# Performance work log

Hardware: AMD Instinct MI355X
Metric: run time of the kernel (lower is better)

The kernel has to match this reference:

```python
import jax, jax.numpy as jnp
import numpy as np

N = 100000
E = 1600000
IN_C = 128
OUT_C = 64
HID = 2 * OUT_C  # 128


def gcn_conv(x, src, dst, W, b, n):
    # PyG GCNConv with add_self_loops=True, symmetric normalization, bias.
    h = x @ W  # [n, d_out] - transform first (PyG order)
    ones = jnp.ones(src.shape[0], dtype=h.dtype)
    deg = jax.ops.segment_sum(ones, dst, num_segments=n)  # includes self-loops -> deg >= 1
    dinv = jax.lax.rsqrt(deg)
    norm = dinv[src] * dinv[dst]  # [E+n]
    msg = h[src] * norm[:, None]  # gather + scale
    return jax.ops.segment_sum(msg, dst, num_segments=n) + b


def setup_inputs() -> dict:
    key = jax.random.key(0)
    ks = jax.random.split(key, 8)
    x = jax.random.normal(ks[0], (N, IN_C), dtype=jnp.float32)
    edge_index = jax.random.randint(ks[1], (2, E), 0, N, dtype=jnp.int64)
    s1 = 1.0 / np.sqrt(IN_C)
    s2 = 1.0 / np.sqrt(HID)
    s3 = 1.0 / np.sqrt(OUT_C)
    W1 = jax.random.normal(ks[2], (IN_C, HID), dtype=jnp.float32) * s1
    b1 = jnp.zeros((HID,), dtype=jnp.float32)
    W2 = jax.random.normal(ks[3], (HID, OUT_C), dtype=jnp.float32) * s2
    b2 = jnp.zeros((OUT_C,), dtype=jnp.float32)
    Wfc = jax.random.normal(ks[4], (OUT_C, OUT_C), dtype=jnp.float32) * s3
    bfc = jax.random.uniform(ks[5], (OUT_C,), dtype=jnp.float32, minval=-s3, maxval=s3)
    return {"x": x, "edge_index": edge_index, "W1": W1, "b1": b1,
            "W2": W2, "b2": b2, "Wfc": Wfc, "bfc": bfc}


def reference(x, edge_index, W1, b1, W2, b2, Wfc, bfc):
    n = x.shape[0]
    loop = jnp.arange(n, dtype=edge_index.dtype)
    src = jnp.concatenate([edge_index[0], loop])  # add self-loops
    dst = jnp.concatenate([edge_index[1], loop])
    h = jax.nn.relu(gcn_conv(x, src, dst, W1, b1, n))
    h = gcn_conv(h, src, dst, W2, b2, n)
    return h @ Wfc + bfc
```

## Files before the change

### kernel.cpp

```cpp
#include <hip/hip_runtime.h>

#define INC  128
#define HIDC 128
#define OUTC 64

#define BSH   8
#define NBMAX 512
#define HB    128
#define TILE  4096
#define CAP   8192

typedef unsigned int  u32;
typedef unsigned short u16;
typedef short bf16x8 __attribute__((ext_vector_type(8)));
typedef float f32x4 __attribute__((ext_vector_type(4)));

static __device__ __forceinline__ u16 f2bf(float f) {
    u32 u = __builtin_bit_cast(u32, f);
    u += 0x7fffu + ((u >> 16) & 1u);
    return (u16)(u >> 16);
}
static __device__ __forceinline__ float bf_lo(u32 u) {
    return __builtin_bit_cast(float, u << 16);
}
static __device__ __forceinline__ float bf_hi(u32 u) {
    return __builtin_bit_cast(float, u & 0xffff0000u);
}


__global__ __launch_bounds__(256) void bhist_kernel(const int* __restrict__ dst,
                                                    int* __restrict__ parts,
                                                    int E, int nb) {
    __shared__ int h[NBMAX];
    for (int i = threadIdx.x; i < NBMAX; i += 256) h[i] = 0;
    __syncthreads();
    const int total = HB * 256;
    for (int e = blockIdx.x * 256 + threadIdx.x; e < E; e += total)
        atomicAdd(&h[dst[e] >> BSH], 1);
    __syncthreads();
    for (int i = threadIdx.x; i < nb; i += 256) parts[i * HB + blockIdx.x] = h[i];
}

__global__ __launch_bounds__(512) void bscan_kernel(const int* __restrict__ parts,
                                                    int* __restrict__ bucketOff, int nb) {
    __shared__ int sums[NBMAX];
    const int tid = threadIdx.x;
    int s = 0;
    if (tid < nb) {
        const int* p = parts + tid * HB;
#pragma unroll 8
        for (int r = 0; r < HB; ++r) s += p[r];
    }
    sums[tid] = s;
    __syncthreads();
    for (int d = 1; d < NBMAX; d <<= 1) {
        int t = sums[tid];
        int a = (tid >= d) ? sums[tid - d] : 0;
        __syncthreads();
        sums[tid] = t + a;
        __syncthreads();
    }
    if (tid < nb) bucketOff[tid] = sums[tid] - s;
    if (tid == NBMAX - 1) bucketOff[nb] = sums[NBMAX - 1];
}

__global__ __launch_bounds__(256) void multisplit_kernel(const int* __restrict__ src,
                                                         const int* __restrict__ dst,
                                                         const int* __restrict__ bucketOff,
                                                         int* __restrict__ gfill,
                                                         int2* __restrict__ binned,
                                                         int E, int nb) {
    __shared__ int hist[NBMAX];
    __shared__ int sbase[NBMAX];
    __shared__ int cursor[NBMAX];
    __shared__ int gposs[NBMAX];
    __shared__ int wsum[4];
    __shared__ int2 buf[TILE];
    const int tid  = threadIdx.x;
    const int base = blockIdx.x * TILE;
    const int cnt  = min(TILE, E - base);

    for (int i = tid; i < NBMAX; i += 256) hist[i] = 0;
    __syncthreads();

    int ls[16], ld[16], dg[16];
#pragma unroll
    for (int k = 0; k < 16; ++k) {
        int idx = tid + k * 256;
        if (idx < cnt) {
            ls[k] = src[base + idx];
            ld[k] = dst[base + idx];
            dg[k] = ld[k] >> BSH;
            atomicAdd(&hist[dg[k]], 1);
        } else dg[k] = -1;
    }
    __syncthreads();
    {
        const int a = hist[2 * tid], b = hist[2 * tid + 1];
        const int s = a + b;
        const int lane = tid & 63;
        int incl = s;
#pragma unroll
        for (int d = 1; d < 64; d <<= 1) {
            int t = __shfl_up(incl, d);
            if (lane >= d) incl += t;
        }
        if (lane == 63) wsum[tid >> 6] = incl;
        __syncthreads();
        const int w = tid >> 6;
        int wbase = 0;
        if (w > 0) wbase += wsum[0];
        if (w > 1) wbase += wsum[1];
        if (w > 2) wbase += wsum[2];
        const int excl = wbase + incl - s;
        sbase[2 * tid] = excl;          cursor[2 * tid] = excl;
        sbase[2 * tid + 1] = excl + a;  cursor[2 * tid + 1] = excl + a;
    }
    __syncthreads();
#pragma unroll
    for (int k = 0; k < 16; ++k) {
        if (dg[k] >= 0) {
            int p = atomicAdd(&cursor[dg[k]], 1);
            buf[p] = make_int2(ls[k], ld[k]);
        }
    }
    __syncthreads();
    for (int d = tid; d < nb; d += 256) {
        int c = cursor[d] - sbase[d];
        gposs[d] = (c > 0) ? atomicAdd(&gfill[d], c) : 0;
    }
    __syncthreads();
    for (int idx = tid; idx < cnt; idx += 256) {
        int2 e = buf[idx];
        int d = e.y >> BSH;
        binned[bucketOff[d] + gposs[d] + (idx - sbase[d])] = e;
    }
}

__global__ __launch_bounds__(256) void csr_build_kernel(const int2* __restrict__ binned,
                                                        const int* __restrict__ bucketOff,
                                                        int* __restrict__ col,
                                                        int* __restrict__ rowptr,
                                                        float* __restrict__ dinv,
                                                        int n, int E) {
    __shared__ int cnt[257];
    __shared__ int excl[256];
    __shared__ int wsum[4];
    __shared__ int colstage[CAP];
    const int tid   = threadIdx.x;
    const int b     = blockIdx.x;
    const int node0 = b << BSH;
    const int nNodes = min(256, n - node0);
    const int e0 = bucketOff[b], e1 = bucketOff[b + 1];
    const int ec = e1 - e0;

    for (int i = tid; i <= 256; i += 256) cnt[i] = 0;
    __syncthreads();
    for (int i = tid; i < ec; i += 256)
        atomicAdd(&cnt[binned[e0 + i].y & 255], 1);
    __syncthreads();
    const int myc = cnt[tid];
    {
        const int lane = tid & 63;
        int incl = myc;
#pragma unroll
        for (int d = 1; d < 64; d <<= 1) {
            int t = __shfl_up(incl, d);
            if (lane >= d) incl += t;
        }
        if (lane == 63) wsum[tid >> 6] = incl;
        __syncthreads();
        const int w = tid >> 6;
        int wbase = 0;
        if (w > 0) wbase += wsum[0];
        if (w > 1) wbase += wsum[1];
        if (w > 2) wbase += wsum[2];
        excl[tid] = wbase + incl - myc;
    }
    __syncthreads();
    if (tid < nNodes) {
        const int node = node0 + tid;
        rowptr[node] = e0 + excl[tid];
        dinv[node] = rsqrtf((float)(myc + 1));
    }
    if (b == 0 && tid == 0) rowptr[n] = E;
    __syncthreads();
    cnt[tid] = excl[tid];
    __syncthreads();
    if (ec <= CAP) {
        for (int i = tid; i < ec; i += 256) {
            int2 e = binned[e0 + i];
            int p = atomicAdd(&cnt[e.y & 255], 1);
            colstage[p] = e.x;
        }
        __syncthreads();
        for (int i = tid; i < ec; i += 256) col[e0 + i] = colstage[i];
    } else {
        for (int i = tid; i < ec; i += 256) {
            int2 e = binned[e0 + i];
            int p = atomicAdd(&cnt[e.y & 255], 1);
            col[e0 + p] = e.x;
        }
    }
}

__global__ __launch_bounds__(256) void fold_kernel(const float* __restrict__ W1,
                                                   const float* __restrict__ W2,
                                                   const float* __restrict__ Wfc,
                                                   const float* __restrict__ b2,
                                                   const float* __restrict__ bfc,
                                                   u16* __restrict__ W1t,
                                                   u16* __restrict__ W2ft,
                                                   float* __restrict__ b2f) {
    int t = blockIdx.x * 256 + threadIdx.x;
    if (t < HIDC * HIDC) {
        int nn = t >> 7, k = t & 127;
        W1t[nn * HIDC + k] = f2bf(W1[k * HIDC + nn]);
    } else if (t < HIDC * HIDC + HIDC * OUTC) {
        int u = t - HIDC * HIDC;
        int i = u >> 6, j = u & 63;
        float s = 0.f;
#pragma unroll 8
        for (int k = 0; k < OUTC; ++k) s = fmaf(W2[i * OUTC + k], Wfc[k * OUTC + j], s);
        W2ft[j * HIDC + i] = f2bf(s);
    } else if (t < HIDC * HIDC + HIDC * OUTC + OUTC) {
        int j = t - HIDC * HIDC - HIDC * OUTC;
        float s = bfc[j];
#pragma unroll 8
        for (int k = 0; k < OUTC; ++k) s = fmaf(b2[k], Wfc[k * OUTC + j], s);
        b2f[j] = s;
    }
}


template <int N, bool AF32>
__global__ __launch_bounds__(256) void mfma_gemm_kernel(const void* __restrict__ Aptr,
                                                        const u16* __restrict__ Wt,
                                                        const float* __restrict__ dinv,
                                                        u16* __restrict__ out, int M) {
    constexpr int K = 128;
    constexpr int NC = N / 16;
    __shared__ u16 Ws[N * K];

    const int tid = threadIdx.x;
    for (int id = tid; id < N * K / 8; id += 256) {
        int nn = id >> 4;
        int c  = id & 15;
        uint4 v = *(const uint4*)(Wt + nn * K + c * 8);
        int slot = (nn << 4) + (c ^ (nn & 7));
        *(uint4*)((char*)Ws + slot * 16) = v;
    }

    const int wave = tid >> 6;
    const int lane = tid & 63;
    const int r0   = blockIdx.x * 64 + wave * 16;
    const int arow = r0 + (lane & 15);
    const int kgrp = lane >> 4;
    __syncthreads();

    f32x4 acc[NC];
#pragma unroll
    for (int nc = 0; nc < NC; ++nc) acc[nc] = f32x4{0.f, 0.f, 0.f, 0.f};

#pragma unroll
    for (int kc = 0; kc < 4; ++kc) {
        bf16x8 af = {0, 0, 0, 0, 0, 0, 0, 0};
        if (arow < M) {
            if constexpr (AF32) {
                const float* ap = (const float*)Aptr + (size_t)arow * K + kc * 32 + kgrp * 8;
                float4 v0 = *(const float4*)ap;
                float4 v1 = *(const float4*)(ap + 4);
                af[0] = (short)f2bf(v0.x); af[1] = (short)f2bf(v0.y);
                af[2] = (short)f2bf(v0.z); af[3] = (short)f2bf(v0.w);
                af[4] = (short)f2bf(v1.x); af[5] = (short)f2bf(v1.y);
                af[6] = (short)f2bf(v1.z); af[7] = (short)f2bf(v1.w);
            } else {
                af = *(const bf16x8*)((const u16*)Aptr + (size_t)arow * K + kc * 32 + kgrp * 8);
            }
        }
#pragma unroll
        for (int nc = 0; nc < NC; ++nc) {
            int nn = nc * 16 + (lane & 15);
            int slot = (nn << 4) + ((kc * 4 + kgrp) ^ (nn & 7));
            bf16x8 bfr = *(const bf16x8*)((const char*)Ws + slot * 16);
            acc[nc] = __builtin_amdgcn_mfma_f32_16x16x32_bf16(af, bfr, acc[nc], 0, 0, 0);
        }
    }
#pragma unroll
    for (int reg = 0; reg < 4; ++reg) {
        int row = r0 + (lane >> 4) * 4 + reg;
        if (row < M) {
            float sc = dinv[row];
#pragma unroll
            for (int nc = 0; nc < NC; ++nc)
                out[(size_t)row * N + nc * 16 + (lane & 15)] = f2bf(acc[nc][reg] * sc);
        }
    }
}


__global__ __launch_bounds__(256) void agg1_kernel(const u32* __restrict__ g,
                                                   const int* __restrict__ rowptr,
                                                   const int* __restrict__ col,
                                                   const float* __restrict__ dinv,
                                                   const float* __restrict__ b1,
                                                   u32* __restrict__ h1, int n) {
    const int wid  = threadIdx.x >> 6;
    const int lane = threadIdx.x & 63;
    const int v = blockIdx.x * 4 + wid;
    if (v >= n) return;
    const int base = rowptr[v], endi = rowptr[v + 1];

    u32 uv = g[(size_t)v * 64 + lane];
    float a0x = bf_lo(uv), a0y = bf_hi(uv);
    float a1x = 0.f, a1y = 0.f, a2x = 0.f, a2y = 0.f, a3x = 0.f, a3y = 0.f;
    float a4x = 0.f, a4y = 0.f, a5x = 0.f, a5y = 0.f, a6x = 0.f, a6y = 0.f, a7x = 0.f, a7y = 0.f;

    for (int c = base; c < endi; c += 64) {
        const int m = min(64, endi - c);
        const int idx = col[c + min(lane, m - 1)];
        for (int i = 0; i < m; i += 8) {
            int u0 = __shfl(idx, i);
            int u1 = __shfl(idx, min(i + 1, m - 1));
            int u2 = __shfl(idx, min(i + 2, m - 1));
            int u3 = __shfl(idx, min(i + 3, m - 1));
            int u4 = __shfl(idx, min(i + 4, m - 1));
            int u5 = __shfl(idx, min(i + 5, m - 1));
            int u6 = __shfl(idx, min(i + 6, m - 1));
            int u7 = __shfl(idx, min(i + 7, m - 1));
            float w1 = (i + 1 < m) ? 1.f : 0.f;
            float w2 = (i + 2 < m) ? 1.f : 0.f;
            float w3 = (i + 3 < m) ? 1.f : 0.f;
            float w4 = (i + 4 < m) ? 1.f : 0.f;
            float w5 = (i + 5 < m) ? 1.f : 0.f;
            float w6 = (i + 6 < m) ? 1.f : 0.f;
            float w7 = (i + 7 < m) ? 1.f : 0.f;
            u32 x0 = g[(size_t)u0 * 64 + lane];
            u32 x1 = g[(size_t)u1 * 64 + lane];
            u32 x2 = g[(size_t)u2 * 64 + lane];
            u32 x3 = g[(size_t)u3 * 64 + lane];
            u32 x4 = g[(size_t)u4 * 64 + lane];
            u32 x5 = g[(size_t)u5 * 64 + lane];
            u32 x6 = g[(size_t)u6 * 64 + lane];
            u32 x7 = g[(size_t)u7 * 64 + lane];
            a0x += bf_lo(x0);                a0y += bf_hi(x0);
            a1x = fmaf(w1, bf_lo(x1), a1x);  a1y = fmaf(w1, bf_hi(x1), a1y);
            a2x = fmaf(w2, bf_lo(x2), a2x);  a2y = fmaf(w2, bf_hi(x2), a2y);
            a3x = fmaf(w3, bf_lo(x3), a3x);  a3y = fmaf(w3, bf_hi(x3), a3y);
            a4x = fmaf(w4, bf_lo(x4), a4x);  a4y = fmaf(w4, bf_hi(x4), a4y);
            a5x = fmaf(w5, bf_lo(x5), a5x);  a5y = fmaf(w5, bf_hi(x5), a5y);
            a6x = fmaf(w6, bf_lo(x6), a6x);  a6y = fmaf(w6, bf_hi(x6), a6y);
            a7x = fmaf(w7, bf_lo(x7), a7x);  a7y = fmaf(w7, bf_hi(x7), a7y);
        }
    }
    float sx = ((a0x + a1x) + (a2x + a3x)) + ((a4x + a5x) + (a6x + a7x));
    float sy = ((a0y + a1y) + (a2y + a3y)) + ((a4y + a5y) + (a6y + a7y));
    const float dv = dinv[v];
    const float2 bb = *(const float2*)&b1[lane * 2];
    float o0 = fmaxf(fmaf(dv, sx, bb.x), 0.f);
    float o1 = fmaxf(fmaf(dv, sy, bb.y), 0.f);
    h1[(size_t)v * 64 + lane] = (u32)f2bf(o0) | ((u32)f2bf(o1) << 16);
}

__global__ __launch_bounds__(256) void agg2_kernel(const u16* __restrict__ g2,
                                                   const int* __restrict__ rowptr,
                                                   const int* __restrict__ col,
                                                   const float* __restrict__ dinv,
                                                   const float* __restrict__ b2f,
                                                   float* __restrict__ out, int n) {
    const int wid  = threadIdx.x >> 6;
    const int lane = threadIdx.x & 63;
    const int v = blockIdx.x * 4 + wid;
    if (v >= n) return;
    const int base = rowptr[v], endi = rowptr[v + 1];

    float a0 = __builtin_bit_cast(float, (u32)g2[(size_t)v * 64 + lane] << 16);
    float a1 = 0.f, a2 = 0.f, a3 = 0.f, a4 = 0.f, a5 = 0.f, a6 = 0.f, a7 = 0.f;

    for (int c = base; c < endi; c += 64) {
        const int m = min(64, endi - c);
        const int idx = col[c + min(lane, m - 1)];
        for (int i = 0; i < m; i += 8) {
            int u0 = __shfl(idx, i);
            int u1 = __shfl(idx, min(i + 1, m - 1));
            int u2 = __shfl(idx, min(i + 2, m - 1));
            int u3 = __shfl(idx, min(i + 3, m - 1));
            int u4 = __shfl(idx, min(i + 4, m - 1));
            int u5 = __shfl(idx, min(i + 5, m - 1));
            int u6 = __shfl(idx, min(i + 6, m - 1));
            int u7 = __shfl(idx, min(i + 7, m - 1));
            float w1 = (i + 1 < m) ? 1.f : 0.f;
            float w2 = (i + 2 < m) ? 1.f : 0.f;
            float w3 = (i + 3 < m) ? 1.f : 0.f;
            float w4 = (i + 4 < m) ? 1.f : 0.f;
            float w5 = (i + 5 < m) ? 1.f : 0.f;
            float w6 = (i + 6 < m) ? 1.f : 0.f;
            float w7 = (i + 7 < m) ? 1.f : 0.f;
            float x0 = __builtin_bit_cast(float, (u32)g2[(size_t)u0 * 64 + lane] << 16);
            float x1 = __builtin_bit_cast(float, (u32)g2[(size_t)u1 * 64 + lane] << 16);
            float x2 = __builtin_bit_cast(float, (u32)g2[(size_t)u2 * 64 + lane] << 16);
            float x3 = __builtin_bit_cast(float, (u32)g2[(size_t)u3 * 64 + lane] << 16);
            float x4 = __builtin_bit_cast(float, (u32)g2[(size_t)u4 * 64 + lane] << 16);
            float x5 = __builtin_bit_cast(float, (u32)g2[(size_t)u5 * 64 + lane] << 16);
            float x6 = __builtin_bit_cast(float, (u32)g2[(size_t)u6 * 64 + lane] << 16);
            float x7 = __builtin_bit_cast(float, (u32)g2[(size_t)u7 * 64 + lane] << 16);
            a0 += x0;
            a1 = fmaf(w1, x1, a1);
            a2 = fmaf(w2, x2, a2);
            a3 = fmaf(w3, x3, a3);
            a4 = fmaf(w4, x4, a4);
            a5 = fmaf(w5, x5, a5);
            a6 = fmaf(w6, x6, a6);
            a7 = fmaf(w7, x7, a7);
        }
    }
    float s = ((a0 + a1) + (a2 + a3)) + ((a4 + a5) + (a6 + a7));
    out[(size_t)v * OUTC + lane] = fmaf(dinv[v], s, b2f[lane]);
}


extern "C" void kernel_launch(void* const* d_in, const int* in_sizes, int n_in,
                              void* d_out, int out_size, void* d_ws, size_t ws_size,
                              hipStream_t stream) {
    const float* x   = (const float*)d_in[0];
    const int*   ei  = (const int*)d_in[1];
    const float* W1  = (const float*)d_in[2];
    const float* b1  = (const float*)d_in[3];
    const float* W2  = (const float*)d_in[4];
    const float* b2  = (const float*)d_in[5];
    const float* Wfc = (const float*)d_in[6];
    const float* bfc = (const float*)d_in[7];
    float* out = (float*)d_out;

    const int n = in_sizes[0] / INC;
    const int E = in_sizes[1] / 2;
    const int* src = ei;
    const int* dst = ei + E;
    const int nb = (n + 255) >> BSH;

    char* w = (char*)d_ws;
    auto alloc = [&](size_t bytes) -> void* {
        void* p = (void*)w;
        w += (bytes + 255) & ~(size_t)255;
        return p;
    };
    int*   rowptr    = (int*)alloc((size_t)(n + 1) * 4);
    float* dinvp     = (float*)alloc((size_t)n * 4);
    int*   col       = (int*)alloc((size_t)E * 4);
    int2*  binned    = (int2*)alloc((size_t)E * 8);
    int*   parts     = (int*)alloc((size_t)NBMAX * HB * 4);
    int*   bucketOff = (int*)alloc((size_t)(nb + 1) * 4);
    int*   gfill     = (int*)alloc((size_t)nb * 4);
    u16*   g         = (u16*)alloc((size_t)n * HIDC * 2);
    u16*   h1        = (u16*)alloc((size_t)n * HIDC * 2);
    u16*   W1t       = (u16*)alloc((size_t)HIDC * HIDC * 2);
    u16*   W2ft      = (u16*)alloc((size_t)OUTC * HIDC * 2);
    float* b2f       = (float*)alloc((size_t)OUTC * 4);

    hipMemsetAsync(gfill, 0, (size_t)nb * 4, stream);

    fold_kernel<<<(HIDC * HIDC + HIDC * OUTC + OUTC + 255) / 256, 256, 0, stream>>>(
        W1, W2, Wfc, b2, bfc, W1t, W2ft, b2f);
    bhist_kernel<<<HB, 256, 0, stream>>>(dst, parts, E, nb);
    bscan_kernel<<<1, NBMAX, 0, stream>>>(parts, bucketOff, nb);
    multisplit_kernel<<<(E + TILE - 1) / TILE, 256, 0, stream>>>(src, dst, bucketOff, gfill, binned, E, nb);
    csr_build_kernel<<<nb, 256, 0, stream>>>(binned, bucketOff, col, rowptr, dinvp, n, E);

    mfma_gemm_kernel<HIDC, true><<<(n + 63) / 64, 256, 0, stream>>>(x, W1t, dinvp, g, n);
    agg1_kernel<<<(n + 3) / 4, 256, 0, stream>>>((const u32*)g, rowptr, col, dinvp, b1, (u32*)h1, n);

    mfma_gemm_kernel<OUTC, false><<<(n + 63) / 64, 256, 0, stream>>>(h1, W2ft, dinvp, g, n);
    agg2_kernel<<<(n + 3) / 4, 256, 0, stream>>>(g, rowptr, col, dinvp, b2f, out, n);
}
```

Baseline: 205.9 us.

## Widen aggregation gathers, add zero sentinel row, pack binned edges to 32-bit

The aggregation kernels now have each lane load 4 bf16 features (8 bytes), with half-waves or quarter-waves handling different neighbors, and sum the partial results with xor shuffles. Padding indices point at a zero sentinel row n, written by the GEMM with scale 0, which replaces the clamped-index and 0/1 weight masking. The binned edge array is packed into one u32 per edge (24-bit src plus 8-bit local dst), halving the traffic between multisplit and CSR build. The packing caps node ids at 2^24, and the wider gathers give fewer independent loads in flight per lane.

```diff
diff --git a/kernel.cpp b/kernel.cpp
--- a/kernel.cpp
+++ b/kernel.cpp
@@ -68,7 +68,7 @@
                                                          const int* __restrict__ dst,
                                                          const int* __restrict__ bucketOff,
                                                          int* __restrict__ gfill,
-                                                         int2* __restrict__ binned,
+                                                         u32* __restrict__ binned,
                                                          int E, int nb) {
     __shared__ int hist[NBMAX];
     __shared__ int sbase[NBMAX];
@@ -133,11 +133,12 @@
     for (int idx = tid; idx < cnt; idx += 256) {
         int2 e = buf[idx];
         int d = e.y >> BSH;
-        binned[bucketOff[d] + gposs[d] + (idx - sbase[d])] = e;
-    }
-}
-
-__global__ __launch_bounds__(256) void csr_build_kernel(const int2* __restrict__ binned,
+        binned[bucketOff[d] + gposs[d] + (idx - sbase[d])] =
+            (u32)e.x | ((u32)(e.y & 255) << 24);
+    }
+}
+
+__global__ __launch_bounds__(256) void csr_build_kernel(const u32* __restrict__ binned,
                                                         const int* __restrict__ bucketOff,
                                                         int* __restrict__ col,
                                                         int* __restrict__ rowptr,
@@ -157,7 +158,7 @@
     for (int i = tid; i <= 256; i += 256) cnt[i] = 0;
     __syncthreads();
     for (int i = tid; i < ec; i += 256)
-        atomicAdd(&cnt[binned[e0 + i].y & 255], 1);
+        atomicAdd(&cnt[binned[e0 + i] >> 24], 1);
     __syncthreads();
     const int myc = cnt[tid];
     {
@@ -189,17 +190,17 @@
     __syncthreads();
     if (ec <= CAP) {
         for (int i = tid; i < ec; i += 256) {
-            int2 e = binned[e0 + i];
-            int p = atomicAdd(&cnt[e.y & 255], 1);
-            colstage[p] = e.x;
+            u32 e = binned[e0 + i];
+            int p = atomicAdd(&cnt[e >> 24], 1);
+            colstage[p] = (int)(e & 0xffffffu);
         }
         __syncthreads();
         for (int i = tid; i < ec; i += 256) col[e0 + i] = colstage[i];
     } else {
         for (int i = tid; i < ec; i += 256) {
-            int2 e = binned[e0 + i];
-            int p = atomicAdd(&cnt[e.y & 255], 1);
-            col[e0 + p] = e.x;
+            u32 e = binned[e0 + i];
+            int p = atomicAdd(&cnt[e >> 24], 1);
+            col[e0 + p] = (int)(e & 0xffffffu);
         }
     }
 }
@@ -289,8 +290,8 @@
 #pragma unroll
     for (int reg = 0; reg < 4; ++reg) {
         int row = r0 + (lane >> 4) * 4 + reg;
-        if (row < M) {
-            float sc = dinv[row];
+        if (row <= M) {
+            float sc = (row < M) ? dinv[row] : 0.f;
 #pragma unroll
             for (int nc = 0; nc < NC; ++nc)
                 out[(size_t)row * N + nc * 16 + (lane & 15)] = f2bf(acc[nc][reg] * sc);
@@ -299,7 +300,7 @@
 }
 
 
-__global__ __launch_bounds__(256) void agg1_kernel(const u32* __restrict__ g,
+__global__ __launch_bounds__(256) void agg1_kernel(const u16* __restrict__ g,
                                                    const int* __restrict__ rowptr,
                                                    const int* __restrict__ col,
                                                    const float* __restrict__ dinv,
@@ -309,57 +310,55 @@
     const int lane = threadIdx.x & 63;
     const int v = blockIdx.x * 4 + wid;
     if (v >= n) return;
+    const int h = lane >> 5;
+    const int r = lane & 31;
     const int base = rowptr[v], endi = rowptr[v + 1];
 
-    u32 uv = g[(size_t)v * 64 + lane];
-    float a0x = bf_lo(uv), a0y = bf_hi(uv);
-    float a1x = 0.f, a1y = 0.f, a2x = 0.f, a2y = 0.f, a3x = 0.f, a3y = 0.f;
-    float a4x = 0.f, a4y = 0.f, a5x = 0.f, a5y = 0.f, a6x = 0.f, a6y = 0.f, a7x = 0.f, a7y = 0.f;
+    float a0 = 0.f, a1 = 0.f, a2 = 0.f, a3 = 0.f;
+    float b0 = 0.f, b1v = 0.f, b2v = 0.f, b3 = 0.f;
+    {
+        uint2 sv = *(const uint2*)(g + ((size_t)v << 7) + (r << 2));
+        if (h == 0) {
+            a0 = bf_lo(sv.x); a1 = bf_hi(sv.x);
+            a2 = bf_lo(sv.y); a3 = bf_hi(sv.y);
+        }
+    }
 
     for (int c = base; c < endi; c += 64) {
         const int m = min(64, endi - c);
-        const int idx = col[c + min(lane, m - 1)];
+        const int idx = (lane < m) ? col[c + lane] : n;
         for (int i = 0; i < m; i += 8) {
-            int u0 = __shfl(idx, i);
-            int u1 = __shfl(idx, min(i + 1, m - 1));
-            int u2 = __shfl(idx, min(i + 2, m - 1));
-            int u3 = __shfl(idx, min(i + 3, m - 1));
-            int u4 = __shfl(idx, min(i + 4, m - 1));
-            int u5 = __shfl(idx, min(i + 5, m - 1));
-            int u6 = __shfl(idx, min(i + 6, m - 1));
-            int u7 = __shfl(idx, min(i + 7, m - 1));
-            float w1 = (i + 1 < m) ? 1.f : 0.f;
-            float w2 = (i + 2 < m) ? 1.f : 0.f;
-            float w3 = (i + 3 < m) ? 1.f : 0.f;
-            float w4 = (i + 4 < m) ? 1.f : 0.f;
-            float w5 = (i + 5 < m) ? 1.f : 0.f;
-            float w6 = (i + 6 < m) ? 1.f : 0.f;
-            float w7 = (i + 7 < m) ? 1.f : 0.f;
-            u32 x0 = g[(size_t)u0 * 64 + lane];
-            u32 x1 = g[(size_t)u1 * 64 + lane];
-            u32 x2 = g[(size_t)u2 * 64 + lane];
-            u32 x3 = g[(size_t)u3 * 64 + lane];
-            u32 x4 = g[(size_t)u4 * 64 + lane];
-            u32 x5 = g[(size_t)u5 * 64 + lane];
-            u32 x6 = g[(size_t)u6 * 64 + lane];
-            u32 x7 = g[(size_t)u7 * 64 + lane];
-            a0x += bf_lo(x0);                a0y += bf_hi(x0);
-            a1x = fmaf(w1, bf_lo(x1), a1x);  a1y = fmaf(w1, bf_hi(x1), a1y);
-            a2x = fmaf(w2, bf_lo(x2), a2x);  a2y = fmaf(w2, bf_hi(x2), a2y);
-            a3x = fmaf(w3, bf_lo(x3), a3x);  a3y = fmaf(w3, bf_hi(x3), a3y);
-            a4x = fmaf(w4, bf_lo(x4), a4x);  a4y = fmaf(w4, bf_hi(x4), a4y);
-            a5x = fmaf(w5, bf_lo(x5), a5x);  a5y = fmaf(w5, bf_hi(x5), a5y);
-            a6x = fmaf(w6, bf_lo(x6), a6x);  a6y = fmaf(w6, bf_hi(x6), a6y);
-            a7x = fmaf(w7, bf_lo(x7), a7x);  a7y = fmaf(w7, bf_hi(x7), a7y);
-        }
-    }
-    float sx = ((a0x + a1x) + (a2x + a3x)) + ((a4x + a5x) + (a6x + a7x));
-    float sy = ((a0y + a1y) + (a2y + a3y)) + ((a4y + a5y) + (a6y + a7y));
-    const float dv = dinv[v];
-    const float2 bb = *(const float2*)&b1[lane * 2];
-    float o0 = fmaxf(fmaf(dv, sx, bb.x), 0.f);
-    float o1 = fmaxf(fmaf(dv, sy, bb.y), 0.f);
-    h1[(size_t)v * 64 + lane] = (u32)f2bf(o0) | ((u32)f2bf(o1) << 16);
+            int u0 = __shfl(idx, i + h);
+            int u1 = __shfl(idx, i + 2 + h);
+            int u2 = __shfl(idx, i + 4 + h);
+            int u3 = __shfl(idx, i + 6 + h);
+            uint2 x0 = *(const uint2*)(g + ((size_t)u0 << 7) + (r << 2));
+            uint2 x1 = *(const uint2*)(g + ((size_t)u1 << 7) + (r << 2));
+            uint2 x2 = *(const uint2*)(g + ((size_t)u2 << 7) + (r << 2));
+            uint2 x3 = *(const uint2*)(g + ((size_t)u3 << 7) + (r << 2));
+            a0 += bf_lo(x0.x); a1 += bf_hi(x0.x); a2 += bf_lo(x0.y); a3 += bf_hi(x0.y);
+            b0 += bf_lo(x1.x); b1v += bf_hi(x1.x); b2v += bf_lo(x1.y); b3 += bf_hi(x1.y);
+            a0 += bf_lo(x2.x); a1 += bf_hi(x2.x); a2 += bf_lo(x2.y); a3 += bf_hi(x2.y);
+            b0 += bf_lo(x3.x); b1v += bf_hi(x3.x); b2v += bf_lo(x3.y); b3 += bf_hi(x3.y);
+        }
+    }
+    float s0 = a0 + b0, s1 = a1 + b1v, s2 = a2 + b2v, s3 = a3 + b3;
+    s0 += __shfl_xor(s0, 32);
+    s1 += __shfl_xor(s1, 32);
+    s2 += __shfl_xor(s2, 32);
+    s3 += __shfl_xor(s3, 32);
+    if (h == 0) {
+        const float dv = dinv[v];
+        const float4 bb = *(const float4*)&b1[r << 2];
+        float o0 = fmaxf(fmaf(dv, s0, bb.x), 0.f);
+        float o1 = fmaxf(fmaf(dv, s1, bb.y), 0.f);
+        float o2 = fmaxf(fmaf(dv, s2, bb.z), 0.f);
+        float o3 = fmaxf(fmaf(dv, s3, bb.w), 0.f);
+        uint2 pk;
+        pk.x = (u32)f2bf(o0) | ((u32)f2bf(o1) << 16);
+        pk.y = (u32)f2bf(o2) | ((u32)f2bf(o3) << 16);
+        *(uint2*)(h1 + ((size_t)v << 6) + (r << 1)) = pk;
+    }
 }
 
 __global__ __launch_bounds__(256) void agg2_kernel(const u16* __restrict__ g2,
@@ -372,50 +371,47 @@
     const int lane = threadIdx.x & 63;
     const int v = blockIdx.x * 4 + wid;
     if (v >= n) return;
+    const int q = lane >> 4;
+    const int r = lane & 15;
     const int base = rowptr[v], endi = rowptr[v + 1];
 
-    float a0 = __builtin_bit_cast(float, (u32)g2[(size_t)v * 64 + lane] << 16);
-    float a1 = 0.f, a2 = 0.f, a3 = 0.f, a4 = 0.f, a5 = 0.f, a6 = 0.f, a7 = 0.f;
+    float a0 = 0.f, a1 = 0.f, a2 = 0.f, a3 = 0.f;
+    float b0 = 0.f, b1v = 0.f, b2v = 0.f, b3 = 0.f;
+    {
+        uint2 sv = *(const uint2*)(g2 + ((size_t)v << 6) + (r << 2));
+        if (q == 0) {
+            a0 = bf_lo(sv.x); a1 = bf_hi(sv.x);
+            a2 = bf_lo(sv.y); a3 = bf_hi(sv.y);
+        }
+    }
 
     for (int c = base; c < endi; c += 64) {
         const int m = min(64, endi - c);
-        const int idx = col[c + min(lane, m - 1)];
+        const int idx = (lane < m) ? col[c + lane] : n;
         for (int i = 0; i < m; i += 8) {
-            int u0 = __shfl(idx, i);
-            int u1 = __shfl(idx, min(i + 1, m - 1));
-            int u2 = __shfl(idx, min(i + 2, m - 1));
-            int u3 = __shfl(idx, min(i + 3, m - 1));
-            int u4 = __shfl(idx, min(i + 4, m - 1));
-            int u5 = __shfl(idx, min(i + 5, m - 1));
-            int u6 = __shfl(idx, min(i + 6, m - 1));
-            int u7 = __shfl(idx, min(i + 7, m - 1));
-            float w1 = (i + 1 < m) ? 1.f : 0.f;
-            float w2 = (i + 2 < m) ? 1.f : 0.f;
-            float w3 = (i + 3 < m) ? 1.f : 0.f;
-            float w4 = (i + 4 < m) ? 1.f : 0.f;
-            float w5 = (i + 5 < m) ? 1.f : 0.f;
-            float w6 = (i + 6 < m) ? 1.f : 0.f;
-            float w7 = (i + 7 < m) ? 1.f : 0.f;
-            float x0 = __builtin_bit_cast(float, (u32)g2[(size_t)u0 * 64 + lane] << 16);
-            float x1 = __builtin_bit_cast(float, (u32)g2[(size_t)u1 * 64 + lane] << 16);
-            float x2 = __builtin_bit_cast(float, (u32)g2[(size_t)u2 * 64 + lane] << 16);
-            float x3 = __builtin_bit_cast(float, (u32)g2[(size_t)u3 * 64 + lane] << 16);
-            float x4 = __builtin_bit_cast(float, (u32)g2[(size_t)u4 * 64 + lane] << 16);
-            float x5 = __builtin_bit_cast(float, (u32)g2[(size_t)u5 * 64 + lane] << 16);
-            float x6 = __builtin_bit_cast(float, (u32)g2[(size_t)u6 * 64 + lane] << 16);
-            float x7 = __builtin_bit_cast(float, (u32)g2[(size_t)u7 * 64 + lane] << 16);
-            a0 += x0;
-            a1 = fmaf(w1, x1, a1);
-            a2 = fmaf(w2, x2, a2);
-            a3 = fmaf(w3, x3, a3);
-            a4 = fmaf(w4, x4, a4);
-            a5 = fmaf(w5, x5, a5);
-            a6 = fmaf(w6, x6, a6);
-            a7 = fmaf(w7, x7, a7);
-        }
-    }
-    float s = ((a0 + a1) + (a2 + a3)) + ((a4 + a5) + (a6 + a7));
-    out[(size_t)v * OUTC + lane] = fmaf(dinv[v], s, b2f[lane]);
+            int u0 = __shfl(idx, i + q);
+            int u1 = __shfl(idx, i + 4 + q);
+            uint2 x0 = *(const uint2*)(g2 + ((size_t)u0 << 6) + (r << 2));
+            uint2 x1 = *(const uint2*)(g2 + ((size_t)u1 << 6) + (r << 2));
+            a0 += bf_lo(x0.x); a1 += bf_hi(x0.x); a2 += bf_lo(x0.y); a3 += bf_hi(x0.y);
+            b0 += bf_lo(x1.x); b1v += bf_hi(x1.x); b2v += bf_lo(x1.y); b3 += bf_hi(x1.y);
+        }
+    }
+    float s0 = a0 + b0, s1 = a1 + b1v, s2 = a2 + b2v, s3 = a3 + b3;
+    s0 += __shfl_xor(s0, 16); s0 += __shfl_xor(s0, 32);
+    s1 += __shfl_xor(s1, 16); s1 += __shfl_xor(s1, 32);
+    s2 += __shfl_xor(s2, 16); s2 += __shfl_xor(s2, 32);
+    s3 += __shfl_xor(s3, 16); s3 += __shfl_xor(s3, 32);
+    if (q == 0) {
+        const float dv = dinv[v];
+        const float4 bb = *(const float4*)&b2f[r << 2];
+        float4 o;
+        o.x = fmaf(dv, s0, bb.x);
+        o.y = fmaf(dv, s1, bb.y);
+        o.z = fmaf(dv, s2, bb.z);
+        o.w = fmaf(dv, s3, bb.w);
+        *(float4*)(out + ((size_t)v << 6) + (r << 2)) = o;
+    }
 }
 
 
@@ -446,12 +442,12 @@
     };
     int*   rowptr    = (int*)alloc((size_t)(n + 1) * 4);
     float* dinvp     = (float*)alloc((size_t)n * 4);
-    int*   col       = (int*)alloc((size_t)E * 4);
-    int2*  binned    = (int2*)alloc((size_t)E * 8);
+    int*   col       = (int*)alloc((size_t)(E + 64) * 4);
+    u32*   binned    = (u32*)alloc((size_t)E * 4);
     int*   parts     = (int*)alloc((size_t)NBMAX * HB * 4);
     int*   bucketOff = (int*)alloc((size_t)(nb + 1) * 4);
     int*   gfill     = (int*)alloc((size_t)nb * 4);
-    u16*   g         = (u16*)alloc((size_t)n * HIDC * 2);
+    u16*   g         = (u16*)alloc((size_t)(n + 1) * HIDC * 2);
     u16*   h1        = (u16*)alloc((size_t)n * HIDC * 2);
     u16*   W1t       = (u16*)alloc((size_t)HIDC * HIDC * 2);
     u16*   W2ft      = (u16*)alloc((size_t)OUTC * HIDC * 2);
@@ -466,9 +462,9 @@
     multisplit_kernel<<<(E + TILE - 1) / TILE, 256, 0, stream>>>(src, dst, bucketOff, gfill, binned, E, nb);
     csr_build_kernel<<<nb, 256, 0, stream>>>(binned, bucketOff, col, rowptr, dinvp, n, E);
 
-    mfma_gemm_kernel<HIDC, true><<<(n + 63) / 64, 256, 0, stream>>>(x, W1t, dinvp, g, n);
-    agg1_kernel<<<(n + 3) / 4, 256, 0, stream>>>((const u32*)g, rowptr, col, dinvp, b1, (u32*)h1, n);
-
-    mfma_gemm_kernel<OUTC, false><<<(n + 63) / 64, 256, 0, stream>>>(h1, W2ft, dinvp, g, n);
+    mfma_gemm_kernel<HIDC, true><<<(n + 64) / 64, 256, 0, stream>>>(x, W1t, dinvp, g, n);
+    agg1_kernel<<<(n + 3) / 4, 256, 0, stream>>>(g, rowptr, col, dinvp, b1, (u32*)h1, n);
+
+    mfma_gemm_kernel<OUTC, false><<<(n + 64) / 64, 256, 0, stream>>>(h1, W2ft, dinvp, g, n);
     agg2_kernel<<<(n + 3) / 4, 256, 0, stream>>>(g, rowptr, col, dinvp, b2f, out, n);
 }
```

Measured after the change: 197.0 us. 1.05x faster.
